# Kernel optimization log

Measured on AMD Instinct MI355X. Metric: run time of the kernel, lower is better.

The kernel has to match this reference:

```python
import jax, jax.numpy as jnp
import numpy as np

D_MODEL = 512
N_STATE = 64
EMB_DIM = 512
LN_EPS = 1e-5


def setup_inputs() -> dict:
    key = jax.random.key(0)
    ks = jax.random.split(key, 12)
    B, L, d, N, e = 8, 2048, D_MODEL, N_STATE, EMB_DIM
    x = jax.random.normal(ks[0], (B, L, d), dtype=jnp.float32)
    emb = jax.random.normal(ks[1], (B, e), dtype=jnp.float32)
    # S4D kernel params
    A_real = -0.5 * jnp.ones((d, N), dtype=jnp.float32)
    A_imag = jnp.pi * jnp.broadcast_to(jnp.arange(N, dtype=jnp.float32)[None, :], (d, N))
    C = jax.random.normal(ks[2], (d, N, 2), dtype=jnp.float32) * 0.5
    dt_min, dt_max = 0.001, 0.1
    log_dt = jax.random.uniform(ks[3], (d,), dtype=jnp.float32) * (np.log(dt_max) - np.log(dt_min)) + np.log(dt_min)
    B_ssm = jnp.ones((d, N), dtype=jnp.float32)  # buffer, treated as constant
    # block params
    D_skip = jax.random.normal(ks[4], (d,), dtype=jnp.float32) * 0.01
    ln_gamma = jnp.ones((d,), dtype=jnp.float32)
    ln_beta = jnp.zeros((d,), dtype=jnp.float32)
    lim_out = 1.0 / np.sqrt(d)
    W_out = jax.random.uniform(ks[5], (2 * d, d), dtype=jnp.float32, minval=-lim_out, maxval=lim_out)
    b_out = jax.random.uniform(ks[6], (2 * d,), dtype=jnp.float32, minval=-lim_out, maxval=lim_out)
    lim_f = 1.0 / np.sqrt(e)
    W_film = jax.random.uniform(ks[7], (2 * d, e), dtype=jnp.float32, minval=-lim_f, maxval=lim_f)
    b_film = jax.random.uniform(ks[8], (2 * d,), dtype=jnp.float32, minval=-lim_f, maxval=lim_f)
    return dict(x=x, emb=emb, A_real=A_real, A_imag=A_imag, C=C, log_dt=log_dt,
                B_ssm=B_ssm, D_skip=D_skip, ln_gamma=ln_gamma, ln_beta=ln_beta,
                W_out=W_out, b_out=b_out, W_film=W_film, b_film=b_film)


def reference(x, emb, A_real, A_imag, C, log_dt, B_ssm, D_skip, ln_gamma, ln_beta,
              W_out, b_out, W_film, b_film):
    Bsz, L, d = x.shape
    residual = x
    # LayerNorm
    mu = jnp.mean(x, axis=-1, keepdims=True)
    var = jnp.mean((x - mu) ** 2, axis=-1, keepdims=True)
    xn = (x - mu) * jax.lax.rsqrt(var + LN_EPS) * ln_gamma + ln_beta
    # S4D kernel: K[d,l] = Re( sum_n (C*B)[d,n] * exp(dt*A)[d,n]**l ) * dt[d]
    dt = jnp.exp(log_dt)                                 # (d,)
    A = A_real + 1j * A_imag                             # (d,N)
    dtA = A * dt[:, None]                                # (d,N)
    Cc = (C[..., 0] + 1j * C[..., 1]) * B_ssm            # (d,N) complex
    l = jnp.arange(L, dtype=jnp.float32)
    powers = jnp.exp(dtA[:, :, None] * l)                # (d,N,L) complex, A_bar**l
    K = jnp.einsum('dn,dnl->dl', Cc, powers).real * dt[:, None]  # (d,L)
    # FFT convolution (circular over 2L -> linear)
    x_t = jnp.transpose(xn, (0, 2, 1))                   # (B,d,L)
    K_f = jnp.fft.rfft(K, n=2 * L)                       # (d,L+1)
    x_f = jnp.fft.rfft(x_t, n=2 * L)                     # (B,d,L+1)
    y = jnp.fft.irfft(K_f[None] * x_f, n=2 * L)[..., :L] # (B,d,L)
    y = y + x_t * D_skip[None, :, None]
    y = jnp.transpose(y, (0, 2, 1))                      # (B,L,d)
    # FiLM conditioning
    film = jax.nn.silu(emb) @ W_film.T + b_film          # (B,2d)
    scale, shift = jnp.split(film, 2, axis=-1)
    y = y * (1.0 + scale[:, None, :]) + shift[:, None, :]
    # out_proj: Linear(d,2d) + GLU
    proj = y @ W_out.T + b_out                           # (B,L,2d)
    a, g = jnp.split(proj, 2, axis=-1)
    y = a * jax.nn.sigmoid(g)
    return residual + y
```

## Files before the change

### kernel.cpp

```cpp
#include <hip/hip_runtime.h>
#include <math.h>

typedef __attribute__((ext_vector_type(8))) short bf8v;
typedef __attribute__((ext_vector_type(4))) float f4v;

union BF8 { bf8v v; unsigned short e[8]; };

__device__ __forceinline__ float bf2f(unsigned short u) {
  union { unsigned int i; float f; } c; c.i = ((unsigned int)u) << 16; return c.f;
}
__device__ __forceinline__ unsigned short f2bf(float f) {
  union { float f; unsigned int i; } c; c.f = f;
  return (unsigned short)((c.i + 0x7fffu + ((c.i >> 16) & 1u)) >> 16);
}
__device__ __forceinline__ void gld16(const unsigned short* g, unsigned short* l) {
  __builtin_amdgcn_global_load_lds(
      (const __attribute__((address_space(1))) unsigned int*)g,
      (__attribute__((address_space(3))) unsigned int*)l, 16, 0, 0);
}

__global__ __launch_bounds__(256) void prelude_kernel(
    const float* __restrict__ emb, const float* __restrict__ Wf,
    const float* __restrict__ bfm, float* __restrict__ film,
    const float* __restrict__ W, unsigned short* __restrict__ Wb,
    const float* __restrict__ A_real, const float* __restrict__ A_imag,
    const float* __restrict__ Cc, const float* __restrict__ log_dt,
    const float* __restrict__ B_ssm, const float* __restrict__ D_skip,
    unsigned short* __restrict__ Pre, unsigned short* __restrict__ Pim,
    unsigned short* __restrict__ Mre, unsigned short* __restrict__ Mim,
    unsigned short* __restrict__ Tt, float* __restrict__ W64r, float* __restrict__ W64i) {
  __shared__ float Ktl[64];
  const int blk = blockIdx.x;
  const int tid = threadIdx.x;
  if (blk < 2048) {
    const int gw = blk * 4 + (tid >> 6);
    const int lane = tid & 63;
    const int b = gw >> 10, j = gw & 1023;
    const float4* ep = (const float4*)(emb + (size_t)b * 512) + lane * 2;
    const float4* wp = (const float4*)(Wf + (size_t)j * 512) + lane * 2;
    float acc = 0.f;
    #pragma unroll
    for (int i = 0; i < 2; i++) {
      const float4 e = ep[i], w = wp[i];
      acc += (e.x / (1.f + __expf(-e.x))) * w.x;
      acc += (e.y / (1.f + __expf(-e.y))) * w.y;
      acc += (e.z / (1.f + __expf(-e.z))) * w.z;
      acc += (e.w / (1.f + __expf(-e.w))) * w.w;
    }
    #pragma unroll
    for (int off = 32; off >= 1; off >>= 1) acc += __shfl_xor(acc, off);
    if (lane == 0) film[(size_t)b * 1024 + j] = acc + bfm[j];
  } else if (blk < 2560) {
    const int i = (blk - 2048) * 256 + tid;
    const float4 v = ((const float4*)W)[i];
    uint2 pk;
    pk.x = (unsigned)f2bf(v.x) | ((unsigned)f2bf(v.y) << 16);
    pk.y = (unsigned)f2bf(v.z) | ((unsigned)f2bf(v.w) << 16);
    ((uint2*)Wb)[i] = pk;
  } else {
    const int d = blk - 2560;
    const float dt = __expf(log_dt[d]);
    const int wv = tid >> 6, n = tid & 63;
    {
      const int dn = d * 64 + n;
      const float ar = dt * A_real[dn], ai = dt * A_imag[dn];
      const float bs = B_ssm[dn] * dt;
      const float c0 = Cc[dn * 2] * bs, c1 = Cc[dn * 2 + 1] * bs;
      #pragma unroll
      for (int i = 0; i < 16; i++) {
        const float tau = (float)(wv * 16 + i);
        const float ex = __expf(ar * tau);
        float sn, cs; __sincosf(ai * tau, &sn, &cs);
        float r = ex * (c0 * cs - c1 * sn);
        #pragma unroll
        for (int off = 32; off >= 1; off >>= 1) r += __shfl_xor(r, off);
        if (n == 0) Ktl[wv * 16 + i] = (wv * 16 + i == 0) ? (r + D_skip[d]) : r;
      }
    }
    __syncthreads();
    for (int g = tid; g < 512; g += 256) {
      const int nn = g >> 3, s0 = (g & 7) * 8;
      const int dn = d * 64 + nn;
      const float ar = dt * A_real[dn], ai = dt * A_imag[dn];
      union { unsigned short s[8]; uint4 u; } pr, pi;
      #pragma unroll
      for (int j = 0; j < 8; j++) {
        const float k = (float)(63 - (s0 + j));
        const float ex = __expf(ar * k);
        float sn, cs; __sincosf(ai * k, &sn, &cs);
        pr.s[j] = f2bf(ex * cs); pi.s[j] = f2bf(ex * sn);
      }
      *(uint4*)(Pre + (size_t)d * 4096 + nn * 64 + s0) = pr.u;
      *(uint4*)(Pim + (size_t)d * 4096 + nn * 64 + s0) = pi.u;
    }
    for (int g = tid; g < 512; g += 256) {
      const int t = g >> 3, n0 = (g & 7) * 8;
      union { unsigned short s[8]; uint4 u; } mr, mi;
      #pragma unroll
      for (int j = 0; j < 8; j++) {
        const int dn = d * 64 + n0 + j;
        const float ar = dt * A_real[dn], ai = dt * A_imag[dn];
        const float bs = B_ssm[dn] * dt;
        const float c0 = Cc[dn * 2] * bs, c1 = Cc[dn * 2 + 1] * bs;
        const float k = (float)(t + 1);
        const float ex = __expf(ar * k);
        float sn, cs; __sincosf(ai * k, &sn, &cs);
        mr.s[j] = f2bf(ex * (c0 * cs - c1 * sn));
        mi.s[j] = f2bf(-ex * (c0 * sn + c1 * cs));
      }
      *(uint4*)(Mre + (size_t)d * 4096 + t * 64 + n0) = mr.u;
      *(uint4*)(Mim + (size_t)d * 4096 + t * 64 + n0) = mi.u;
    }
    for (int g = tid; g < 512; g += 256) {
      const int t = g >> 3, s0 = (g & 7) * 8;
      union { unsigned short s[8]; uint4 u; } tv;
      #pragma unroll
      for (int j = 0; j < 8; j++) {
        const int s = s0 + j;
        tv.s[j] = (s <= t) ? f2bf(Ktl[t - s]) : (unsigned short)0;
      }
      *(uint4*)(Tt + (size_t)d * 4096 + t * 64 + s0) = tv.u;
    }
    if (tid < 64) {
      const int dn = d * 64 + tid;
      const float ex = __expf(dt * A_real[dn] * 64.f);
      float sn, cs; __sincosf(dt * A_imag[dn] * 64.f, &sn, &cs);
      W64r[d * 64 + tid] = ex * cs;
      W64i[d * 64 + tid] = ex * sn;
    }
  }
}

__global__ __launch_bounds__(256) void lnt_kernel(const float* __restrict__ x,
    const float* __restrict__ gamma, const float* __restrict__ beta,
    unsigned short* __restrict__ xT) {
  __shared__ __align__(16) unsigned short t[16 * 520];
  const int r0 = blockIdx.x * 16;
  const int tid = threadIdx.x, wv = tid >> 6, lane = tid & 63;
  const float4* gp = (const float4*)gamma + lane * 2;
  const float4* bp = (const float4*)beta  + lane * 2;
  const float4 g0 = gp[0], g1 = gp[1], bb0 = bp[0], bb1 = bp[1];
  #pragma unroll
  for (int i = 0; i < 4; i++) {
    const int r = wv * 4 + i;
    const float4* xr = (const float4*)(x + (size_t)(r0 + r) * 512) + lane * 2;
    const float4 v0 = xr[0], v1 = xr[1];
    float s  = v0.x + v0.y + v0.z + v0.w + v1.x + v1.y + v1.z + v1.w;
    float sq = v0.x*v0.x + v0.y*v0.y + v0.z*v0.z + v0.w*v0.w
             + v1.x*v1.x + v1.y*v1.y + v1.z*v1.z + v1.w*v1.w;
    #pragma unroll
    for (int off = 32; off >= 1; off >>= 1) {
      s  += __shfl_xor(s, off);
      sq += __shfl_xor(sq, off);
    }
    const float mu   = s * (1.f / 512.f);
    const float var  = sq * (1.f / 512.f) - mu * mu;
    const float rstd = rsqrtf(var + 1e-5f);
    uint4 pk;
    pk.x = (unsigned)f2bf((v0.x - mu) * rstd * g0.x + bb0.x)
         | ((unsigned)f2bf((v0.y - mu) * rstd * g0.y + bb0.y) << 16);
    pk.y = (unsigned)f2bf((v0.z - mu) * rstd * g0.z + bb0.z)
         | ((unsigned)f2bf((v0.w - mu) * rstd * g0.w + bb0.w) << 16);
    pk.z = (unsigned)f2bf((v1.x - mu) * rstd * g1.x + bb1.x)
         | ((unsigned)f2bf((v1.y - mu) * rstd * g1.y + bb1.y) << 16);
    pk.w = (unsigned)f2bf((v1.z - mu) * rstd * g1.z + bb1.z)
         | ((unsigned)f2bf((v1.w - mu) * rstd * g1.w + bb1.w) << 16);
    *(uint4*)&t[r * 520 + lane * 8] = pk;
  }
  __syncthreads();
  const int p = tid;
  union { unsigned short s[8]; uint4 u; } a0, a1, b0, b1;
  #pragma unroll
  for (int r = 0; r < 8; r++) {
    const unsigned v = *(const unsigned*)&t[r * 520 + p * 2];
    a0.s[r] = (unsigned short)(v & 0xffffu);
    b0.s[r] = (unsigned short)(v >> 16);
  }
  #pragma unroll
  for (int r = 0; r < 8; r++) {
    const unsigned v = *(const unsigned*)&t[(r + 8) * 520 + p * 2];
    a1.s[r] = (unsigned short)(v & 0xffffu);
    b1.s[r] = (unsigned short)(v >> 16);
  }
  unsigned short* o0 = xT + (size_t)(2 * p) * 16384 + r0;
  *(uint4*)o0 = a0.u; *(uint4*)(o0 + 8) = a1.u;
  unsigned short* o1 = xT + (size_t)(2 * p + 1) * 16384 + r0;
  *(uint4*)o1 = b0.u; *(uint4*)(o1 + 8) = b1.u;
}

__global__ __launch_bounds__(256) void tr_kernel(const unsigned short* __restrict__ in,
    unsigned short* __restrict__ out, int R, int C) {
  __shared__ __align__(16) unsigned short t[64 * 72];
  const int c0 = blockIdx.x * 64, r0 = blockIdx.y * 64;
  const int tid = threadIdx.x;
  #pragma unroll
  for (int i = 0; i < 2; i++) {
    const int idx = tid + i * 256;
    const int r = idx >> 3, q = idx & 7;
    const uint4 v = *(const uint4*)(in + (size_t)(r0 + r) * C + c0 + q * 8);
    *(uint4*)&t[r * 72 + ((q ^ (r >> 3)) * 8)] = v;
  }
  __syncthreads();
  #pragma unroll
  for (int i = 0; i < 2; i++) {
    const int idx = tid + i * 256;
    const int c = idx >> 3, g = idx & 7;
    union { unsigned short s[8]; uint4 u; } pk;
    #pragma unroll
    for (int j = 0; j < 8; j++)
      pk.s[j] = t[(g * 8 + j) * 72 + (((c >> 3) ^ g) * 8) + (c & 7)];
    *(uint4*)(out + (size_t)(c0 + c) * R + r0 + g * 8) = pk.u;
  }
}

__global__ __launch_bounds__(256, 2) void ssm_kernel(
    const unsigned short* __restrict__ xT,
    const unsigned short* __restrict__ Pre, const unsigned short* __restrict__ Pim,
    const unsigned short* __restrict__ Mre, const unsigned short* __restrict__ Mim,
    const unsigned short* __restrict__ Tt,
    const float* __restrict__ W64r, const float* __restrict__ W64i,
    const float* __restrict__ film, unsigned short* __restrict__ y2) {
  extern __shared__ char smem[];
  unsigned short* Pr = (unsigned short*)smem;
  unsigned short* Pi = Pr + 64 * 68;
  unsigned short* Mr = Pi + 64 * 68;
  unsigned short* Mi = Mr + 64 * 68;
  unsigned short* Tl = Mi + 64 * 68;
  unsigned int*   Eb = (unsigned int*)(Tl + 64 * 68);

  const int bx = blockIdx.x;
  const int d = bx & 511, h = bx >> 9;
  const int tid = threadIdx.x;
  const int wv = tid >> 6, lane = tid & 63;
  const int n15 = lane & 15, quad = lane >> 4;
  const int j0 = wv * 32;
  const int jg0 = h * 128;
  const size_t dtab = (size_t)d * 4096;

  {
    const unsigned short* gt[5] = {Pre + dtab, Pim + dtab, Mre + dtab, Mim + dtab, Tt + dtab};
    unsigned short* lt[5] = {Pr, Pi, Mr, Mi, Tl};
    #pragma unroll
    for (int i = 0; i < 10; i++) {
      const int idx = tid + i * 256;
      const int tb = idx >> 9, r = (idx >> 3) & 63, g = idx & 7;
      const uint4 v = *(const uint4*)(gt[tb] + r * 64 + g * 8);
      *(uint4*)&lt[tb][r * 68 + g * 8] = v;
    }
  }
  bf8v Xf[2][2];
  #pragma unroll
  for (int ct = 0; ct < 2; ct++)
    #pragma unroll
    for (int kq = 0; kq < 2; kq++)
      Xf[ct][kq] = *(const bf8v*)(xT + (size_t)d * 16384 +
                                  (jg0 + j0 + ct * 16 + n15) * 64 + kq * 32 + quad * 8);
  __syncthreads();

  {
    f4v Er[4][2], Ei[4][2];
    #pragma unroll
    for (int a = 0; a < 4; a++)
      #pragma unroll
      for (int b2 = 0; b2 < 2; b2++) { Er[a][b2] = (f4v){0,0,0,0}; Ei[a][b2] = (f4v){0,0,0,0}; }
    #pragma unroll
    for (int mt = 0; mt < 4; mt++)
      #pragma unroll
      for (int kq = 0; kq < 2; kq++) {
        const bf8v pr = *(const bf8v*)&Pr[(mt * 16 + n15) * 68 + kq * 32 + quad * 8];
        const bf8v pi = *(const bf8v*)&Pi[(mt * 16 + n15) * 68 + kq * 32 + quad * 8];
        #pragma unroll
        for (int ct = 0; ct < 2; ct++) {
          Er[mt][ct] = __builtin_amdgcn_mfma_f32_16x16x32_bf16(pr, Xf[ct][kq], Er[mt][ct], 0, 0, 0);
          Ei[mt][ct] = __builtin_amdgcn_mfma_f32_16x16x32_bf16(pi, Xf[ct][kq], Ei[mt][ct], 0, 0, 0);
        }
      }
    #pragma unroll
    for (int mt = 0; mt < 4; mt++)
      #pragma unroll
      for (int ct = 0; ct < 2; ct++)
        #pragma unroll
        for (int i = 0; i < 4; i++) {
          const int row = mt * 16 + quad * 4 + i;
          const int col = j0 + ct * 16 + n15;
          Eb[row * 131 + col] =
              (unsigned)f2bf(Er[mt][ct][i]) | ((unsigned)f2bf(Ei[mt][ct][i]) << 16);
        }
  }
  __syncthreads();

  {
    const int n = lane, bp = wv;
    const float wre = W64r[d * 64 + n], wim = W64i[d * 64 + n];
    unsigned int* row = &Eb[n * 131 + bp * 32];
    float str = 0.f, sti = 0.f;
    #pragma unroll
    for (int c = 0; c < 32; c++) {
      const unsigned u = row[c];
      row[c] = (unsigned)f2bf(str) | ((unsigned)f2bf(sti) << 16);
      const float er = bf2f((unsigned short)(u & 0xffffu));
      const float ei = bf2f((unsigned short)(u >> 16));
      const float nr = er + wre * str - wim * sti;
      const float ni = ei + wre * sti + wim * str;
      str = nr; sti = ni;
    }
  }
  __syncthreads();

  f4v Y[4][2];
  #pragma unroll
  for (int a = 0; a < 4; a++)
    #pragma unroll
    for (int b2 = 0; b2 < 2; b2++) Y[a][b2] = (f4v){0,0,0,0};

  #pragma unroll
  for (int mt = 0; mt < 4; mt++)
    #pragma unroll
    for (int kq = 0; kq < 2; kq++) {
      const bf8v tf = *(const bf8v*)&Tl[(mt * 16 + n15) * 68 + kq * 32 + quad * 8];
      #pragma unroll
      for (int ct = 0; ct < 2; ct++)
        Y[mt][ct] = __builtin_amdgcn_mfma_f32_16x16x32_bf16(tf, Xf[ct][kq], Y[mt][ct], 0, 0, 0);
    }

  #pragma unroll
  for (int kq = 0; kq < 2; kq++) {
    BF8 ir[2], ii[2];
    #pragma unroll
    for (int ct = 0; ct < 2; ct++)
      #pragma unroll
      for (int jj = 0; jj < 8; jj++) {
        const unsigned u = Eb[(kq * 32 + quad * 8 + jj) * 131 + (j0 + ct * 16 + n15)];
        ir[ct].e[jj] = (unsigned short)(u & 0xffffu);
        ii[ct].e[jj] = (unsigned short)(u >> 16);
      }
    #pragma unroll
    for (int mt = 0; mt < 4; mt++) {
      const bf8v mr = *(const bf8v*)&Mr[(mt * 16 + n15) * 68 + kq * 32 + quad * 8];
      const bf8v mi = *(const bf8v*)&Mi[(mt * 16 + n15) * 68 + kq * 32 + quad * 8];
      #pragma unroll
      for (int ct = 0; ct < 2; ct++) {
        Y[mt][ct] = __builtin_amdgcn_mfma_f32_16x16x32_bf16(mr, ir[ct].v, Y[mt][ct], 0, 0, 0);
        Y[mt][ct] = __builtin_amdgcn_mfma_f32_16x16x32_bf16(mi, ii[ct].v, Y[mt][ct], 0, 0, 0);
      }
    }
  }

  #pragma unroll
  for (int ct = 0; ct < 2; ct++) {
    const int jglob = jg0 + j0 + ct * 16 + n15;
    const int b = jglob >> 5;
    const float scl = 1.f + film[b * 1024 + d];
    const float shf = film[b * 1024 + 512 + d];
    #pragma unroll
    for (int mt = 0; mt < 4; mt++) {
      union { unsigned short s[4]; uint2 u; } pk;
      #pragma unroll
      for (int i = 0; i < 4; i++)
        pk.s[i] = f2bf(fmaf(Y[mt][ct][i], scl, shf));
      *(uint2*)(y2 + (size_t)d * 16384 + jglob * 64 + mt * 16 + quad * 4) = pk.u;
    }
  }
}

__global__ __launch_bounds__(256, 3) void gemm_kernel(
    const unsigned short* __restrict__ y2n, const unsigned short* __restrict__ Wb,
    const float* __restrict__ bo, const float* __restrict__ x,
    float* __restrict__ out) {
  __shared__ __align__(16) unsigned short Al[128 * 64];
  __shared__ __align__(16) unsigned short Bl[128 * 64];
  const int m0 = blockIdx.x * 128, ct = blockIdx.y;
  const int tid = threadIdx.x;
  const int wv = tid >> 6, lane = tid & 63;
  const int n15 = lane & 15, quad = lane >> 4;
  const int sr = lane >> 3;
  const int sk = ((lane & 7) ^ sr) * 8;

  f4v acc[2][8];
  #pragma unroll
  for (int mi = 0; mi < 2; mi++)
    #pragma unroll
    for (int t4 = 0; t4 < 8; t4++) acc[mi][t4] = (f4v){0.f, 0.f, 0.f, 0.f};

  for (int kk = 0; kk < 8; kk++) {
    #pragma unroll
    for (int c = 0; c < 4; c++) {
      const int row = wv * 32 + c * 8 + sr;
      gld16(y2n + (size_t)(m0 + row) * 512 + kk * 64 + sk, Al + wv * 2048 + c * 512);
      const int cg = (row < 64) ? (ct * 64 + row) : (512 + ct * 64 + (row - 64));
      gld16(Wb + (size_t)cg * 512 + kk * 64 + sk, Bl + wv * 2048 + c * 512);
    }
    __syncthreads();
    #pragma unroll
    for (int kq = 0; kq < 2; kq++) {
      const int r0 = wv * 32 + n15;
      const int r1 = r0 + 16;
      const bf8v a0 = *(const bf8v*)&Al[r0 * 64 + (((kq * 4 + quad) ^ (r0 & 7)) * 8)];
      const bf8v a1 = *(const bf8v*)&Al[r1 * 64 + (((kq * 4 + quad) ^ (r1 & 7)) * 8)];
      #pragma unroll
      for (int t4 = 0; t4 < 8; t4++) {
        const int rb = t4 * 16 + n15;
        const bf8v bb = *(const bf8v*)&Bl[rb * 64 + (((kq * 4 + quad) ^ (rb & 7)) * 8)];
        acc[0][t4] = __builtin_amdgcn_mfma_f32_16x16x32_bf16(a0, bb, acc[0][t4], 0, 0, 0);
        acc[1][t4] = __builtin_amdgcn_mfma_f32_16x16x32_bf16(a1, bb, acc[1][t4], 0, 0, 0);
      }
    }
    __syncthreads();
  }
  #pragma unroll
  for (int mi = 0; mi < 2; mi++) {
    const int mrow = m0 + wv * 32 + mi * 16 + quad * 4;
    #pragma unroll
    for (int t4 = 0; t4 < 4; t4++) {
      const int c = ct * 64 + t4 * 16 + n15;
      const float ba = bo[c], bg = bo[512 + c];
      #pragma unroll
      for (int i = 0; i < 4; i++) {
        const size_t off = (size_t)(mrow + i) * 512 + c;
        const float av = acc[mi][t4][i] + ba;
        const float gv = acc[mi][t4 + 4][i] + bg;
        out[off] = x[off] + av * (1.f / (1.f + __expf(-gv)));
      }
    }
  }
}

extern "C" void kernel_launch(void* const* d_in, const int* in_sizes, int n_in,
                              void* d_out, int out_size, void* d_ws, size_t ws_size,
                              hipStream_t stream) {
  const float* x      = (const float*)d_in[0];
  const float* emb    = (const float*)d_in[1];
  const float* A_real = (const float*)d_in[2];
  const float* A_imag = (const float*)d_in[3];
  const float* C      = (const float*)d_in[4];
  const float* log_dt = (const float*)d_in[5];
  const float* B_ssm  = (const float*)d_in[6];
  const float* D_skip = (const float*)d_in[7];
  const float* gamma  = (const float*)d_in[8];
  const float* beta   = (const float*)d_in[9];
  const float* W_out  = (const float*)d_in[10];
  const float* b_out  = (const float*)d_in[11];
  const float* W_film = (const float*)d_in[12];
  const float* b_film = (const float*)d_in[13];
  float* out = (float*)d_out;

  char* ws = (char*)d_ws;
  size_t o = 0;
  float*          film = (float*)(ws + o);          o += 32768;
  unsigned short* xT   = (unsigned short*)(ws + o); o += 16777216;
  unsigned short* Wb   = (unsigned short*)(ws + o); o += 1048576;
  unsigned short* Pre  = (unsigned short*)(ws + o); o += 4194304;
  unsigned short* Pim  = (unsigned short*)(ws + o); o += 4194304;
  unsigned short* Mre  = (unsigned short*)(ws + o); o += 4194304;
  unsigned short* Mim  = (unsigned short*)(ws + o); o += 4194304;
  unsigned short* Tt   = (unsigned short*)(ws + o); o += 4194304;
  float*          W64r = (float*)(ws + o);          o += 131072;
  float*          W64i = (float*)(ws + o);          o += 131072;
  unsigned short* y2   = (unsigned short*)(ws + o); o += 16777216;
  unsigned short* y2n  = (unsigned short*)(ws + o); o += 16777216;

  prelude_kernel<<<dim3(3072), dim3(256), 0, stream>>>(
      emb, W_film, b_film, film, W_out, Wb,
      A_real, A_imag, C, log_dt, B_ssm, D_skip,
      Pre, Pim, Mre, Mim, Tt, W64r, W64i);
  lnt_kernel<<<dim3(1024), dim3(256), 0, stream>>>(x, gamma, beta, xT);
  ssm_kernel<<<dim3(1024), dim3(256), 77056, stream>>>(xT, Pre, Pim, Mre, Mim, Tt,
                                                       W64r, W64i, film, y2);
  tr_kernel<<<dim3(256, 8), dim3(256), 0, stream>>>(y2, y2n, 512, 16384);
  gemm_kernel<<<dim3(128, 8), dim3(256), 0, stream>>>(y2n, Wb, b_out, x, out);
}
```

Baseline: 193.3 us.

## Fuse LayerNorm into prelude, merge SSM halves per block, enlarge GEMM M-tile

```diff
diff --git a/kernel.cpp b/kernel.cpp
--- a/kernel.cpp
+++ b/kernel.cpp
@@ -28,8 +28,10 @@
     const float* __restrict__ B_ssm, const float* __restrict__ D_skip,
     unsigned short* __restrict__ Pre, unsigned short* __restrict__ Pim,
     unsigned short* __restrict__ Mre, unsigned short* __restrict__ Mim,
-    unsigned short* __restrict__ Tt, float* __restrict__ W64r, float* __restrict__ W64i) {
-  __shared__ float Ktl[64];
+    unsigned short* __restrict__ Tt, float* __restrict__ W64r, float* __restrict__ W64i,
+    const float* __restrict__ x, const float* __restrict__ gamma,
+    const float* __restrict__ beta, unsigned short* __restrict__ xT) {
+  __shared__ __align__(16) char sh[16 * 520 * 2];
   const int blk = blockIdx.x;
   const int tid = threadIdx.x;
   if (blk < 2048) {
@@ -57,7 +59,8 @@
     pk.x = (unsigned)f2bf(v.x) | ((unsigned)f2bf(v.y) << 16);
     pk.y = (unsigned)f2bf(v.z) | ((unsigned)f2bf(v.w) << 16);
     ((uint2*)Wb)[i] = pk;
-  } else {
+  } else if (blk < 3072) {
+    float* Ktl = (float*)sh;
     const int d = blk - 2560;
     const float dt = __expf(log_dt[d]);
     const int wv = tid >> 6, n = tid & 63;
@@ -128,64 +131,60 @@
       W64r[d * 64 + tid] = ex * cs;
       W64i[d * 64 + tid] = ex * sn;
     }
-  }
-}
-
-__global__ __launch_bounds__(256) void lnt_kernel(const float* __restrict__ x,
-    const float* __restrict__ gamma, const float* __restrict__ beta,
-    unsigned short* __restrict__ xT) {
-  __shared__ __align__(16) unsigned short t[16 * 520];
-  const int r0 = blockIdx.x * 16;
-  const int tid = threadIdx.x, wv = tid >> 6, lane = tid & 63;
-  const float4* gp = (const float4*)gamma + lane * 2;
-  const float4* bp = (const float4*)beta  + lane * 2;
-  const float4 g0 = gp[0], g1 = gp[1], bb0 = bp[0], bb1 = bp[1];
-  #pragma unroll
-  for (int i = 0; i < 4; i++) {
-    const int r = wv * 4 + i;
-    const float4* xr = (const float4*)(x + (size_t)(r0 + r) * 512) + lane * 2;
-    const float4 v0 = xr[0], v1 = xr[1];
-    float s  = v0.x + v0.y + v0.z + v0.w + v1.x + v1.y + v1.z + v1.w;
-    float sq = v0.x*v0.x + v0.y*v0.y + v0.z*v0.z + v0.w*v0.w
-             + v1.x*v1.x + v1.y*v1.y + v1.z*v1.z + v1.w*v1.w;
-    #pragma unroll
-    for (int off = 32; off >= 1; off >>= 1) {
-      s  += __shfl_xor(s, off);
-      sq += __shfl_xor(sq, off);
-    }
-    const float mu   = s * (1.f / 512.f);
-    const float var  = sq * (1.f / 512.f) - mu * mu;
-    const float rstd = rsqrtf(var + 1e-5f);
-    uint4 pk;
-    pk.x = (unsigned)f2bf((v0.x - mu) * rstd * g0.x + bb0.x)
-         | ((unsigned)f2bf((v0.y - mu) * rstd * g0.y + bb0.y) << 16);
-    pk.y = (unsigned)f2bf((v0.z - mu) * rstd * g0.z + bb0.z)
-         | ((unsigned)f2bf((v0.w - mu) * rstd * g0.w + bb0.w) << 16);
-    pk.z = (unsigned)f2bf((v1.x - mu) * rstd * g1.x + bb1.x)
-         | ((unsigned)f2bf((v1.y - mu) * rstd * g1.y + bb1.y) << 16);
-    pk.w = (unsigned)f2bf((v1.z - mu) * rstd * g1.z + bb1.z)
-         | ((unsigned)f2bf((v1.w - mu) * rstd * g1.w + bb1.w) << 16);
-    *(uint4*)&t[r * 520 + lane * 8] = pk;
-  }
-  __syncthreads();
-  const int p = tid;
-  union { unsigned short s[8]; uint4 u; } a0, a1, b0, b1;
-  #pragma unroll
-  for (int r = 0; r < 8; r++) {
-    const unsigned v = *(const unsigned*)&t[r * 520 + p * 2];
-    a0.s[r] = (unsigned short)(v & 0xffffu);
-    b0.s[r] = (unsigned short)(v >> 16);
-  }
-  #pragma unroll
-  for (int r = 0; r < 8; r++) {
-    const unsigned v = *(const unsigned*)&t[(r + 8) * 520 + p * 2];
-    a1.s[r] = (unsigned short)(v & 0xffffu);
-    b1.s[r] = (unsigned short)(v >> 16);
-  }
-  unsigned short* o0 = xT + (size_t)(2 * p) * 16384 + r0;
-  *(uint4*)o0 = a0.u; *(uint4*)(o0 + 8) = a1.u;
-  unsigned short* o1 = xT + (size_t)(2 * p + 1) * 16384 + r0;
-  *(uint4*)o1 = b0.u; *(uint4*)(o1 + 8) = b1.u;
+  } else {
+    unsigned short* t = (unsigned short*)sh;
+    const int r0 = (blk - 3072) * 16;
+    const int wv = tid >> 6, lane = tid & 63;
+    const float4* gp = (const float4*)gamma + lane * 2;
+    const float4* bp = (const float4*)beta  + lane * 2;
+    const float4 g0 = gp[0], g1 = gp[1], bb0 = bp[0], bb1 = bp[1];
+    #pragma unroll
+    for (int i = 0; i < 4; i++) {
+      const int r = wv * 4 + i;
+      const float4* xr = (const float4*)(x + (size_t)(r0 + r) * 512) + lane * 2;
+      const float4 v0 = xr[0], v1 = xr[1];
+      float s  = v0.x + v0.y + v0.z + v0.w + v1.x + v1.y + v1.z + v1.w;
+      float sq = v0.x*v0.x + v0.y*v0.y + v0.z*v0.z + v0.w*v0.w
+               + v1.x*v1.x + v1.y*v1.y + v1.z*v1.z + v1.w*v1.w;
+      #pragma unroll
+      for (int off = 32; off >= 1; off >>= 1) {
+        s  += __shfl_xor(s, off);
+        sq += __shfl_xor(sq, off);
+      }
+      const float mu   = s * (1.f / 512.f);
+      const float var  = sq * (1.f / 512.f) - mu * mu;
+      const float rstd = rsqrtf(var + 1e-5f);
+      uint4 pk;
+      pk.x = (unsigned)f2bf((v0.x - mu) * rstd * g0.x + bb0.x)
+           | ((unsigned)f2bf((v0.y - mu) * rstd * g0.y + bb0.y) << 16);
+      pk.y = (unsigned)f2bf((v0.z - mu) * rstd * g0.z + bb0.z)
+           | ((unsigned)f2bf((v0.w - mu) * rstd * g0.w + bb0.w) << 16);
+      pk.z = (unsigned)f2bf((v1.x - mu) * rstd * g1.x + bb1.x)
+           | ((unsigned)f2bf((v1.y - mu) * rstd * g1.y + bb1.y) << 16);
+      pk.w = (unsigned)f2bf((v1.z - mu) * rstd * g1.z + bb1.z)
+           | ((unsigned)f2bf((v1.w - mu) * rstd * g1.w + bb1.w) << 16);
+      *(uint4*)&t[r * 520 + lane * 8] = pk;
+    }
+    __syncthreads();
+    const int p = tid;
+    union { unsigned short s[8]; uint4 u; } a0, a1, b0, b1;
+    #pragma unroll
+    for (int r = 0; r < 8; r++) {
+      const unsigned v = *(const unsigned*)&t[r * 520 + p * 2];
+      a0.s[r] = (unsigned short)(v & 0xffffu);
+      b0.s[r] = (unsigned short)(v >> 16);
+    }
+    #pragma unroll
+    for (int r = 0; r < 8; r++) {
+      const unsigned v = *(const unsigned*)&t[(r + 8) * 520 + p * 2];
+      a1.s[r] = (unsigned short)(v & 0xffffu);
+      b1.s[r] = (unsigned short)(v >> 16);
+    }
+    unsigned short* o0 = xT + (size_t)(2 * p) * 16384 + r0;
+    *(uint4*)o0 = a0.u; *(uint4*)(o0 + 8) = a1.u;
+    unsigned short* o1 = xT + (size_t)(2 * p + 1) * 16384 + r0;
+    *(uint4*)o1 = b0.u; *(uint4*)(o1 + 8) = b1.u;
+  }
 }
 
 __global__ __launch_bounds__(256) void tr_kernel(const unsigned short* __restrict__ in,
@@ -228,13 +227,11 @@
   unsigned short* Tl = Mi + 64 * 68;
   unsigned int*   Eb = (unsigned int*)(Tl + 64 * 68);
 
-  const int bx = blockIdx.x;
-  const int d = bx & 511, h = bx >> 9;
+  const int d = blockIdx.x;
   const int tid = threadIdx.x;
   const int wv = tid >> 6, lane = tid & 63;
   const int n15 = lane & 15, quad = lane >> 4;
   const int j0 = wv * 32;
-  const int jg0 = h * 128;
   const size_t dtab = (size_t)d * 4096;
 
   {
@@ -248,178 +245,195 @@
       *(uint4*)&lt[tb][r * 68 + g * 8] = v;
     }
   }
-  bf8v Xf[2][2];
-  #pragma unroll
-  for (int ct = 0; ct < 2; ct++)
-    #pragma unroll
-    for (int kq = 0; kq < 2; kq++)
-      Xf[ct][kq] = *(const bf8v*)(xT + (size_t)d * 16384 +
-                                  (jg0 + j0 + ct * 16 + n15) * 64 + kq * 32 + quad * 8);
+  bf8v Xf[2][2][2];
+  #pragma unroll
+  for (int h = 0; h < 2; h++)
+    #pragma unroll
+    for (int ct = 0; ct < 2; ct++)
+      #pragma unroll
+      for (int kq = 0; kq < 2; kq++)
+        Xf[h][ct][kq] = *(const bf8v*)(xT + (size_t)d * 16384 +
+            (h * 128 + j0 + ct * 16 + n15) * 64 + kq * 32 + quad * 8);
   __syncthreads();
 
-  {
-    f4v Er[4][2], Ei[4][2];
+  #pragma unroll
+  for (int h = 0; h < 2; h++) {
+    const int jg0 = h * 128;
+    {
+      f4v Er[4][2], Ei[4][2];
+      #pragma unroll
+      for (int a = 0; a < 4; a++)
+        #pragma unroll
+        for (int b2 = 0; b2 < 2; b2++) { Er[a][b2] = (f4v){0,0,0,0}; Ei[a][b2] = (f4v){0,0,0,0}; }
+      #pragma unroll
+      for (int mt = 0; mt < 4; mt++)
+        #pragma unroll
+        for (int kq = 0; kq < 2; kq++) {
+          const bf8v pr = *(const bf8v*)&Pr[(mt * 16 + n15) * 68 + kq * 32 + quad * 8];
+          const bf8v pi = *(const bf8v*)&Pi[(mt * 16 + n15) * 68 + kq * 32 + quad * 8];
+          #pragma unroll
+          for (int ct = 0; ct < 2; ct++) {
+            Er[mt][ct] = __builtin_amdgcn_mfma_f32_16x16x32_bf16(pr, Xf[h][ct][kq], Er[mt][ct], 0, 0, 0);
+            Ei[mt][ct] = __builtin_amdgcn_mfma_f32_16x16x32_bf16(pi, Xf[h][ct][kq], Ei[mt][ct], 0, 0, 0);
+          }
+        }
+      #pragma unroll
+      for (int mt = 0; mt < 4; mt++)
+        #pragma unroll
+        for (int ct = 0; ct < 2; ct++)
+          #pragma unroll
+          for (int i = 0; i < 4; i++) {
+            const int row = mt * 16 + quad * 4 + i;
+            const int col = j0 + ct * 16 + n15;
+            Eb[row * 131 + col] =
+                (unsigned)f2bf(Er[mt][ct][i]) | ((unsigned)f2bf(Ei[mt][ct][i]) << 16);
+          }
+    }
+    __syncthreads();
+
+    {
+      const int n = lane, bp = wv;
+      const float wre = W64r[d * 64 + n], wim = W64i[d * 64 + n];
+      unsigned int* row = &Eb[n * 131 + bp * 32];
+      float str = 0.f, sti = 0.f;
+      #pragma unroll
+      for (int c = 0; c < 32; c++) {
+        const unsigned u = row[c];
+        row[c] = (unsigned)f2bf(str) | ((unsigned)f2bf(sti) << 16);
+        const float er = bf2f((unsigned short)(u & 0xffffu));
+        const float ei = bf2f((unsigned short)(u >> 16));
+        const float nr = er + wre * str - wim * sti;
+        const float ni = ei + wre * sti + wim * str;
+        str = nr; sti = ni;
+      }
+    }
+    __syncthreads();
+
+    f4v Y[4][2];
     #pragma unroll
     for (int a = 0; a < 4; a++)
       #pragma unroll
-      for (int b2 = 0; b2 < 2; b2++) { Er[a][b2] = (f4v){0,0,0,0}; Ei[a][b2] = (f4v){0,0,0,0}; }
+      for (int b2 = 0; b2 < 2; b2++) Y[a][b2] = (f4v){0,0,0,0};
+
     #pragma unroll
     for (int mt = 0; mt < 4; mt++)
       #pragma unroll
       for (int kq = 0; kq < 2; kq++) {
-        const bf8v pr = *(const bf8v*)&Pr[(mt * 16 + n15) * 68 + kq * 32 + quad * 8];
-        const bf8v pi = *(const bf8v*)&Pi[(mt * 16 + n15) * 68 + kq * 32 + quad * 8];
+        const bf8v tf = *(const bf8v*)&Tl[(mt * 16 + n15) * 68 + kq * 32 + quad * 8];
+        #pragma unroll
+        for (int ct = 0; ct < 2; ct++)
+          Y[mt][ct] = __builtin_amdgcn_mfma_f32_16x16x32_bf16(tf, Xf[h][ct][kq], Y[mt][ct], 0, 0, 0);
+      }
+
+    #pragma unroll
+    for (int kq = 0; kq < 2; kq++) {
+      BF8 ir[2], ii[2];
+      #pragma unroll
+      for (int ct = 0; ct < 2; ct++)
+        #pragma unroll
+        for (int jj = 0; jj < 8; jj++) {
+          const unsigned u = Eb[(kq * 32 + quad * 8 + jj) * 131 + (j0 + ct * 16 + n15)];
+          ir[ct].e[jj] = (unsigned short)(u & 0xffffu);
+          ii[ct].e[jj] = (unsigned short)(u >> 16);
+        }
+      #pragma unroll
+      for (int mt = 0; mt < 4; mt++) {
+        const bf8v mr = *(const bf8v*)&Mr[(mt * 16 + n15) * 68 + kq * 32 + quad * 8];
+        const bf8v mi = *(const bf8v*)&Mi[(mt * 16 + n15) * 68 + kq * 32 + quad * 8];
         #pragma unroll
         for (int ct = 0; ct < 2; ct++) {
-          Er[mt][ct] = __builtin_amdgcn_mfma_f32_16x16x32_bf16(pr, Xf[ct][kq], Er[mt][ct], 0, 0, 0);
-          Ei[mt][ct] = __builtin_amdgcn_mfma_f32_16x16x32_bf16(pi, Xf[ct][kq], Ei[mt][ct], 0, 0, 0);
+          Y[mt][ct] = __builtin_amdgcn_mfma_f32_16x16x32_bf16(mr, ir[ct].v, Y[mt][ct], 0, 0, 0);
+          Y[mt][ct] = __builtin_amdgcn_mfma_f32_16x16x32_bf16(mi, ii[ct].v, Y[mt][ct], 0, 0, 0);
         }
       }
-    #pragma unroll
-    for (int mt = 0; mt < 4; mt++)
-      #pragma unroll
-      for (int ct = 0; ct < 2; ct++)
-        #pragma unroll
-        for (int i = 0; i < 4; i++) {
-          const int row = mt * 16 + quad * 4 + i;
-          const int col = j0 + ct * 16 + n15;
-          Eb[row * 131 + col] =
-              (unsigned)f2bf(Er[mt][ct][i]) | ((unsigned)f2bf(Ei[mt][ct][i]) << 16);
-        }
-  }
-  __syncthreads();
-
-  {
-    const int n = lane, bp = wv;
-    const float wre = W64r[d * 64 + n], wim = W64i[d * 64 + n];
-    unsigned int* row = &Eb[n * 131 + bp * 32];
-    float str = 0.f, sti = 0.f;
-    #pragma unroll
-    for (int c = 0; c < 32; c++) {
-      const unsigned u = row[c];
-      row[c] = (unsigned)f2bf(str) | ((unsigned)f2bf(sti) << 16);
-      const float er = bf2f((unsigned short)(u & 0xffffu));
-      const float ei = bf2f((unsigned short)(u >> 16));
-      const float nr = er + wre * str - wim * sti;
-      const float ni = ei + wre * sti + wim * str;
-      str = nr; sti = ni;
-    }
-  }
-  __syncthreads();
-
-  f4v Y[4][2];
-  #pragma unroll
-  for (int a = 0; a < 4; a++)
-    #pragma unroll
-    for (int b2 = 0; b2 < 2; b2++) Y[a][b2] = (f4v){0,0,0,0};
-
-  #pragma unroll
-  for (int mt = 0; mt < 4; mt++)
-    #pragma unroll
-    for (int kq = 0; kq < 2; kq++) {
-      const bf8v tf = *(const bf8v*)&Tl[(mt * 16 + n15) * 68 + kq * 32 + quad * 8];
-      #pragma unroll
-      for (int ct = 0; ct < 2; ct++)
-        Y[mt][ct] = __builtin_amdgcn_mfma_f32_16x16x32_bf16(tf, Xf[ct][kq], Y[mt][ct], 0, 0, 0);
-    }
-
-  #pragma unroll
-  for (int kq = 0; kq < 2; kq++) {
-    BF8 ir[2], ii[2];
-    #pragma unroll
-    for (int ct = 0; ct < 2; ct++)
-      #pragma unroll
-      for (int jj = 0; jj < 8; jj++) {
-        const unsigned u = Eb[(kq * 32 + quad * 8 + jj) * 131 + (j0 + ct * 16 + n15)];
-        ir[ct].e[jj] = (unsigned short)(u & 0xffffu);
-        ii[ct].e[jj] = (unsigned short)(u >> 16);
-      }
-    #pragma unroll
-    for (int mt = 0; mt < 4; mt++) {
-      const bf8v mr = *(const bf8v*)&Mr[(mt * 16 + n15) * 68 + kq * 32 + quad * 8];
-      const bf8v mi = *(const bf8v*)&Mi[(mt * 16 + n15) * 68 + kq * 32 + quad * 8];
-      #pragma unroll
-      for (int ct = 0; ct < 2; ct++) {
-        Y[mt][ct] = __builtin_amdgcn_mfma_f32_16x16x32_bf16(mr, ir[ct].v, Y[mt][ct], 0, 0, 0);
-        Y[mt][ct] = __builtin_amdgcn_mfma_f32_16x16x32_bf16(mi, ii[ct].v, Y[mt][ct], 0, 0, 0);
-      }
-    }
-  }
-
-  #pragma unroll
-  for (int ct = 0; ct < 2; ct++) {
-    const int jglob = jg0 + j0 + ct * 16 + n15;
-    const int b = jglob >> 5;
-    const float scl = 1.f + film[b * 1024 + d];
-    const float shf = film[b * 1024 + 512 + d];
-    #pragma unroll
-    for (int mt = 0; mt < 4; mt++) {
-      union { unsigned short s[4]; uint2 u; } pk;
-      #pragma unroll
-      for (int i = 0; i < 4; i++)
-        pk.s[i] = f2bf(fmaf(Y[mt][ct][i], scl, shf));
-      *(uint2*)(y2 + (size_t)d * 16384 + jglob * 64 + mt * 16 + quad * 4) = pk.u;
-    }
-  }
-}
-
-__global__ __launch_bounds__(256, 3) void gemm_kernel(
+    }
+
+    #pragma unroll
+    for (int ct = 0; ct < 2; ct++) {
+      const int jglob = jg0 + j0 + ct * 16 + n15;
+      const int b = jglob >> 5;
+      const float scl = 1.f + film[b * 1024 + d];
+      const float shf = film[b * 1024 + 512 + d];
+      #pragma unroll
+      for (int mt = 0; mt < 4; mt++) {
+        union { unsigned short s[4]; uint2 u; } pk;
+        #pragma unroll
+        for (int i = 0; i < 4; i++)
+          pk.s[i] = f2bf(fmaf(Y[mt][ct][i], scl, shf));
+        *(uint2*)(y2 + (size_t)d * 16384 + jglob * 64 + mt * 16 + quad * 4) = pk.u;
+      }
+    }
+    if (h == 0) __syncthreads();
+  }
+}
+
+__global__ __launch_bounds__(256) void gemm_kernel(
     const unsigned short* __restrict__ y2n, const unsigned short* __restrict__ Wb,
     const float* __restrict__ bo, const float* __restrict__ x,
     float* __restrict__ out) {
-  __shared__ __align__(16) unsigned short Al[128 * 64];
+  __shared__ __align__(16) unsigned short Al[256 * 64];
   __shared__ __align__(16) unsigned short Bl[128 * 64];
-  const int m0 = blockIdx.x * 128, ct = blockIdx.y;
+  const int m0 = blockIdx.x * 256, cp0 = blockIdx.y * 64;
   const int tid = threadIdx.x;
   const int wv = tid >> 6, lane = tid & 63;
   const int n15 = lane & 15, quad = lane >> 4;
-  const int sr = lane >> 3;
-  const int sk = ((lane & 7) ^ sr) * 8;
-
-  f4v acc[2][8];
-  #pragma unroll
-  for (int mi = 0; mi < 2; mi++)
-    #pragma unroll
-    for (int t4 = 0; t4 < 8; t4++) acc[mi][t4] = (f4v){0.f, 0.f, 0.f, 0.f};
+  const int lr = lane >> 3;
+  const int lg = lane & 7;
+  const int sg = (lg ^ lr) * 8;
+
+  f4v acc[4][8];
+  #pragma unroll
+  for (int mt = 0; mt < 4; mt++)
+    #pragma unroll
+    for (int t4 = 0; t4 < 8; t4++) acc[mt][t4] = (f4v){0.f, 0.f, 0.f, 0.f};
 
   for (int kk = 0; kk < 8; kk++) {
     #pragma unroll
-    for (int c = 0; c < 4; c++) {
-      const int row = wv * 32 + c * 8 + sr;
-      gld16(y2n + (size_t)(m0 + row) * 512 + kk * 64 + sk, Al + wv * 2048 + c * 512);
-      const int cg = (row < 64) ? (ct * 64 + row) : (512 + ct * 64 + (row - 64));
-      gld16(Wb + (size_t)cg * 512 + kk * 64 + sk, Bl + wv * 2048 + c * 512);
+    for (int i = 0; i < 8; i++) {
+      const int row = wv * 64 + i * 8 + lr;
+      gld16(y2n + (size_t)(m0 + row) * 512 + kk * 64 + sg, Al + (wv * 64 + i * 8) * 64);
+    }
+    #pragma unroll
+    for (int i = 0; i < 4; i++) {
+      const int row = wv * 32 + i * 8 + lr;
+      const int cg = (row < 64) ? (cp0 + row) : (512 + cp0 + row - 64);
+      gld16(Wb + (size_t)cg * 512 + kk * 64 + sg, Bl + (wv * 32 + i * 8) * 64);
     }
     __syncthreads();
     #pragma unroll
     for (int kq = 0; kq < 2; kq++) {
-      const int r0 = wv * 32 + n15;
-      const int r1 = r0 + 16;
-      const bf8v a0 = *(const bf8v*)&Al[r0 * 64 + (((kq * 4 + quad) ^ (r0 & 7)) * 8)];
-      const bf8v a1 = *(const bf8v*)&Al[r1 * 64 + (((kq * 4 + quad) ^ (r1 & 7)) * 8)];
+      bf8v av[4], bv[8];
+      #pragma unroll
+      for (int mt = 0; mt < 4; mt++) {
+        const int row = wv * 64 + mt * 16 + n15;
+        av[mt] = *(const bf8v*)&Al[row * 64 + (((kq * 4 + quad) ^ (row & 7)) * 8)];
+      }
       #pragma unroll
       for (int t4 = 0; t4 < 8; t4++) {
-        const int rb = t4 * 16 + n15;
-        const bf8v bb = *(const bf8v*)&Bl[rb * 64 + (((kq * 4 + quad) ^ (rb & 7)) * 8)];
-        acc[0][t4] = __builtin_amdgcn_mfma_f32_16x16x32_bf16(a0, bb, acc[0][t4], 0, 0, 0);
-        acc[1][t4] = __builtin_amdgcn_mfma_f32_16x16x32_bf16(a1, bb, acc[1][t4], 0, 0, 0);
-      }
-    }
-    __syncthreads();
-  }
-  #pragma unroll
-  for (int mi = 0; mi < 2; mi++) {
-    const int mrow = m0 + wv * 32 + mi * 16 + quad * 4;
+        const int row = t4 * 16 + n15;
+        bv[t4] = *(const bf8v*)&Bl[row * 64 + (((kq * 4 + quad) ^ (row & 7)) * 8)];
+      }
+      #pragma unroll
+      for (int mt = 0; mt < 4; mt++)
+        #pragma unroll
+        for (int t4 = 0; t4 < 8; t4++)
+          acc[mt][t4] = __builtin_amdgcn_mfma_f32_16x16x32_bf16(av[mt], bv[t4], acc[mt][t4], 0, 0, 0);
+    }
+    __syncthreads();
+  }
+  #pragma unroll
+  for (int mt = 0; mt < 4; mt++) {
+    const int mrow = m0 + wv * 64 + mt * 16 + quad * 4;
     #pragma unroll
     for (int t4 = 0; t4 < 4; t4++) {
-      const int c = ct * 64 + t4 * 16 + n15;
+      const int c = cp0 + t4 * 16 + n15;
       const float ba = bo[c], bg = bo[512 + c];
       #pragma unroll
       for (int i = 0; i < 4; i++) {
         const size_t off = (size_t)(mrow + i) * 512 + c;
-        const float av = acc[mi][t4][i] + ba;
-        const float gv = acc[mi][t4 + 4][i] + bg;
-        out[off] = x[off] + av * (1.f / (1.f + __expf(-gv)));
+        const float av2 = acc[mt][t4][i] + ba;
+        const float gv = acc[mt][t4 + 4][i] + bg;
+        out[off] = x[off] + av2 * (1.f / (1.f + __expf(-gv)));
       }
     }
   }
@@ -459,13 +473,13 @@
   unsigned short* y2   = (unsigned short*)(ws + o); o += 16777216;
   unsigned short* y2n  = (unsigned short*)(ws + o); o += 16777216;
 
-  prelude_kernel<<<dim3(3072), dim3(256), 0, stream>>>(
+  prelude_kernel<<<dim3(4096), dim3(256), 0, stream>>>(
       emb, W_film, b_film, film, W_out, Wb,
       A_real, A_imag, C, log_dt, B_ssm, D_skip,
-      Pre, Pim, Mre, Mim, Tt, W64r, W64i);
-  lnt_kernel<<<dim3(1024), dim3(256), 0, stream>>>(x, gamma, beta, xT);
-  ssm_kernel<<<dim3(1024), dim3(256), 77056, stream>>>(xT, Pre, Pim, Mre, Mim, Tt,
-                                                       W64r, W64i, film, y2);
+      Pre, Pim, Mre, Mim, Tt, W64r, W64i,
+      x, gamma, beta, xT);
+  ssm_kernel<<<dim3(512), dim3(256), 77056, stream>>>(xT, Pre, Pim, Mre, Mim, Tt,
+                                                      W64r, W64i, film, y2);
   tr_kernel<<<dim3(256, 8), dim3(256), 0, stream>>>(y2, y2n, 512, 16384);
-  gemm_kernel<<<dim3(128, 8), dim3(256), 0, stream>>>(y2n, Wb, b_out, x, out);
-}
+  gemm_kernel<<<dim3(64, 8), dim3(256), 0, stream>>>(y2n, Wb, b_out, x, out);
+}
```

Measured after the change: 196.1 us. About the same (+1.4%).
